# Optimization experiments

Hardware: AMD Instinct MI355X
Metric: run time of the kernel (lower is better)

The kernel has to match this reference:

```python
import jax, jax.numpy as jnp
import numpy as np
from jax import lax

B, T, H, W, C = 2, 32, 64, 64, 64
K, KT = 7, 5


def kernel_to_freq_3d(kernel, T, H, W):
    # kernel: (C, k_t, k_h, k_w) -> (C, T, H, W) complex freq (circularly centered)
    Cc, k_t, k_h, k_w = kernel.shape
    t_idx = (jnp.arange(k_t) - k_t // 2) % T
    h_idx = (jnp.arange(k_h) - k_h // 2) % H
    w_idx = (jnp.arange(k_w) - k_w // 2) % W
    tt, th, tw = jnp.meshgrid(t_idx, h_idx, w_idx, indexing='ij')
    padded = jnp.zeros((Cc, T, H, W), dtype=kernel.dtype).at[:, tt, th, tw].set(kernel)
    return jnp.fft.fftn(padded, axes=(1, 2, 3))


def heinsen_scan_log(log_coeffs, log_values):
    def op(left, right):
        a_l, b_l = left
        a_r, b_r = right
        return (a_l + a_r, jnp.logaddexp(a_r + b_l, b_r))
    _, log_h = lax.associative_scan(op, (log_coeffs, log_values), axis=0)
    return log_h


def setup_inputs() -> dict:
    key = jax.random.key(0)
    ks = jax.random.split(key, 9)
    dense_scale = 1.0 / np.sqrt(C)
    kern_scale = 1.0 / np.sqrt(KT * K * K)
    return {
        'x': jax.random.normal(ks[0], (B, T, H, W, C), jnp.float32),
        'gate_w': jax.random.normal(ks[1], (C, C), jnp.float32) * dense_scale,
        'gate_b': jnp.zeros((C,), jnp.float32),
        'hidden_w': jax.random.normal(ks[2], (C, C), jnp.float32) * dense_scale,
        'hidden_b': jnp.zeros((C,), jnp.float32),
        'gate_kernel': jax.random.normal(ks[3], (C, KT, K, K), jnp.float32) * kern_scale,
        'hidden_kernel': jax.random.normal(ks[4], (C, KT, K, K), jnp.float32) * kern_scale,
        'out_w': jax.random.normal(ks[5], (C, C), jnp.float32) * dense_scale,
        'out_b': jnp.zeros((C,), jnp.float32),
    }


def reference(x, gate_w, gate_b, hidden_w, hidden_b, gate_kernel, hidden_kernel, out_w, out_b):
    Bx, Tx, Hx, Wx, Cx = x.shape
    gate_proj = jnp.einsum('bthwc,cd->bthwd', x, gate_w) + gate_b
    hidden_proj = jnp.einsum('bthwc,cd->bthwd', x, hidden_w) + hidden_b
    # kernels to frequency domain, channel-last: (T, H, W, C)
    gk_f = kernel_to_freq_3d(gate_kernel, Tx, Hx, Wx).transpose(1, 2, 3, 0)
    hk_f = kernel_to_freq_3d(hidden_kernel, Tx, Hx, Wx).transpose(1, 2, 3, 0)
    gate_f = jnp.fft.fftn(gate_proj, axes=(1, 2, 3))
    hidden_f = jnp.fft.fftn(hidden_proj, axes=(1, 2, 3))
    gate_spatial = jnp.fft.ifftn(gate_f * gk_f[None], axes=(1, 2, 3)).real
    hidden_spatial = jnp.fft.ifftn(hidden_f * hk_f[None], axes=(1, 2, 3)).real
    # minGRU in log space: h_t = (1-z_t) h_{t-1} + z_t * h~_t
    log_forget = -jax.nn.softplus(gate_spatial)       # log(1 - z)
    log_update = -jax.nn.softplus(-gate_spatial)      # log(z)
    log_hidden = jnp.log(hidden_spatial ** 2 + 1e-06)
    log_values = log_update + log_hidden
    # scan over T (move T to axis 0)
    log_h_seq = heinsen_scan_log(
        log_forget.transpose(1, 0, 2, 3, 4), log_values.transpose(1, 0, 2, 3, 4))
    h = jnp.exp(log_h_seq.transpose(1, 0, 2, 3, 4))
    out = jnp.einsum('bthwc,cd->bthwd', h, out_w) + out_b
    return out.astype(jnp.float32)
```

## Files before the change

### kernel.cpp

```cpp
#include <hip/hip_runtime.h>
#include <hip/hip_fp16.h>

#define NELEM 16777216

typedef _Float16 f16x8 __attribute__((ext_vector_type(8)));
typedef _Float16 h2v  __attribute__((ext_vector_type(2)));
typedef float f32x4 __attribute__((ext_vector_type(4)));

static __device__ __forceinline__ void pk_fma_sv(uint& d, uint a_s, uint b_v) {
    asm("v_pk_fma_f16 %0, %1, %2, %0" : "+v"(d) : "s"(a_s), "v"(b_v));
}

__global__ __launch_bounds__(256) void proj2_kernel(
    const float* __restrict__ x,
    const float* __restrict__ wg, const float* __restrict__ bg,
    const float* __restrict__ wh, const float* __restrict__ bh,
    uint* __restrict__ pg, uint* __restrict__ ph)
{
    __shared__ __align__(16) _Float16 sX[128 * 64];
    __shared__ __align__(16) _Float16 sWT[2][64 * 64];
    const int tid = threadIdx.x;
    const int row0 = (int)blockIdx.x * 128;

    #pragma unroll
    for (int kci = 0; kci < 4; ++kci) {
        const int chunk = tid + kci * 256;
        const int r = chunk >> 3, q = chunk & 7;
        const float* gp = x + (long long)(row0 + r) * 64 + q * 8;
        const float4 v0 = *reinterpret_cast<const float4*>(gp);
        const float4 v1 = *reinterpret_cast<const float4*>(gp + 4);
        f16x8 hv;
        hv[0] = (_Float16)v0.x; hv[1] = (_Float16)v0.y; hv[2] = (_Float16)v0.z; hv[3] = (_Float16)v0.w;
        hv[4] = (_Float16)v1.x; hv[5] = (_Float16)v1.y; hv[6] = (_Float16)v1.z; hv[7] = (_Float16)v1.w;
        *reinterpret_cast<f16x8*>(&sX[r * 64 + ((q ^ (r & 7)) * 8)]) = hv;
    }
    {
        const int d = tid & 63;
        const int cb = (tid >> 6) * 16;
        #pragma unroll
        for (int i = 0; i < 16; ++i) {
            const int c = cb + i;
            const int off = d * 64 + (((c >> 3) ^ (d & 7)) * 8) + (c & 7);
            sWT[0][off] = (_Float16)wg[c * 64 + d];
            sWT[1][off] = (_Float16)wh[c * 64 + d];
        }
    }
    __syncthreads();

    const int wv = tid >> 6, lm = tid & 15, lg = (tid & 63) >> 4;
    f16x8 bf[2][4][2];
    #pragma unroll
    for (int nt = 0; nt < 4; ++nt) {
        const int d = nt * 16 + lm;
        #pragma unroll
        for (int s = 0; s < 2; ++s) {
            const int off = d * 64 + (((s * 4 + lg) ^ (d & 7)) * 8);
            bf[0][nt][s] = *reinterpret_cast<const f16x8*>(&sWT[0][off]);
            bf[1][nt][s] = *reinterpret_cast<const f16x8*>(&sWT[1][off]);
        }
    }
    f32x4 acc[2][2][4];
    #pragma unroll
    for (int m = 0; m < 2; ++m)
        #pragma unroll
        for (int mt = 0; mt < 2; ++mt)
            #pragma unroll
            for (int nt = 0; nt < 4; ++nt)
                acc[m][mt][nt] = (f32x4){0.f, 0.f, 0.f, 0.f};

    #pragma unroll
    for (int mt = 0; mt < 2; ++mt) {
        const int r = wv * 32 + mt * 16 + lm;
        const f16x8 a0 = *reinterpret_cast<const f16x8*>(&sX[r * 64 + ((lg ^ (r & 7)) * 8)]);
        const f16x8 a1 = *reinterpret_cast<const f16x8*>(&sX[r * 64 + (((4 + lg) ^ (r & 7)) * 8)]);
        #pragma unroll
        for (int nt = 0; nt < 4; ++nt) {
            acc[0][mt][nt] = __builtin_amdgcn_mfma_f32_16x16x32_f16(a0, bf[0][nt][0], acc[0][mt][nt], 0, 0, 0);
            acc[0][mt][nt] = __builtin_amdgcn_mfma_f32_16x16x32_f16(a1, bf[0][nt][1], acc[0][mt][nt], 0, 0, 0);
            acc[1][mt][nt] = __builtin_amdgcn_mfma_f32_16x16x32_f16(a0, bf[1][nt][0], acc[1][mt][nt], 0, 0, 0);
            acc[1][mt][nt] = __builtin_amdgcn_mfma_f32_16x16x32_f16(a1, bf[1][nt][1], acc[1][mt][nt], 0, 0, 0);
        }
    }
    #pragma unroll
    for (int nt = 0; nt < 4; ++nt) {
        const int col = nt * 16 + lm;
        const int pr  = col >> 1;
        const float bgv = bg[col], bhv = bh[col];
        #pragma unroll
        for (int mt = 0; mt < 2; ++mt) {
            const int rb = row0 + wv * 32 + mt * 16 + lg * 4;
            uint pk0[4], pk1[4];
            #pragma unroll
            for (int i = 0; i < 4; ++i) {
                const float v0 = acc[0][mt][nt][i] + bgv;
                const float p0 = __shfl_xor(v0, 1);
                const float v1 = acc[1][mt][nt][i] + bhv;
                const float p1 = __shfl_xor(v1, 1);
                h2v a, c;
                a[0] = (_Float16)((lm & 1) ? p0 : v0); a[1] = (_Float16)((lm & 1) ? v0 : p0);
                c[0] = (_Float16)((lm & 1) ? p1 : v1); c[1] = (_Float16)((lm & 1) ? v1 : p1);
                pk0[i] = __builtin_bit_cast(uint, a);
                pk1[i] = __builtin_bit_cast(uint, c);
            }
            if (!(lm & 1)) {
                *reinterpret_cast<uint4*>(pg + pr * 262144 + rb) = make_uint4(pk0[0], pk0[1], pk0[2], pk0[3]);
                *reinterpret_cast<uint4*>(ph + pr * 262144 + rb) = make_uint4(pk1[0], pk1[1], pk1[2], pk1[3]);
            }
        }
    }
}

__global__ __launch_bounds__(256) void tapconv_kernel(
    const float* __restrict__ gk, const float* __restrict__ hk, uint* __restrict__ taps)
{
    const int i = blockIdx.x * 256 + threadIdx.x;
    if (i >= 17920) return;
    const int kw = i & 7;
    int r = i >> 3;
    const int kth = r % 35;  r /= 35;
    const int p = r & 31;
    const int mat = r >> 5;
    if (kw >= 7) { taps[i] = 0u; return; }
    const float* K = mat ? hk : gk;
    const int tap = kth * 7 + kw;
    h2v hv;
    hv[0] = (_Float16)K[(2 * p) * 245 + tap];
    hv[1] = (_Float16)K[(2 * p + 1) * 245 + tap];
    taps[i] = __builtin_bit_cast(uint, hv);
}

__global__ __launch_bounds__(256) void conv3d_dual_kernel(
    const uint* __restrict__ inG, uint* __restrict__ outG,
    const uint* __restrict__ inH, uint* __restrict__ outH,
    const uint* __restrict__ taps)
{
    const int bid = (int)blockIdx.x;
    const int l = ((bid & 7) << 9) | (bid >> 3);
    const int tile = l & 3;
    const int pgrp = (l >> 2) & 7;
    const int t    = (l >> 5) & 31;
    const int b    = (l >> 10) & 1;
    const int mat  = (l >> 11) & 1;
    const int wave = threadIdx.x >> 6;
    const int lane = threadIdx.x & 63;
    const int h0 = (tile >> 1) * 32, w0 = (tile & 1) * 32;
    const int pair = pgrp * 4 + wave;

    const uint* in = mat ? inH : inG;
    uint* out      = mat ? outH : outG;

    const int iy = lane >> 3, ix = lane & 7;

    const int tapOff = __builtin_amdgcn_readfirstlane((mat * 32 + pair) * 280);
    const uint* tb = taps + tapOff;
    const int pbOff = __builtin_amdgcn_readfirstlane(pair * 262144 + b * 131072);

    int colu[3];
    #pragma unroll
    for (int m = 0; m < 3; ++m) colu[m] = (w0 + 4 * ix - 4 + 4 * m) & 63;

    uint tot[4][4];
    #pragma unroll
    for (int o = 0; o < 4; ++o)
        #pragma unroll
        for (int j = 0; j < 4; ++j) tot[o][j] = 0u;

    #pragma unroll 1
    for (int kt = 0; kt < 5; ++kt) {
        const int tin = (t - kt + 2) & 31;
        const uint* pin = in + pbOff + tin * 4096;
        const uint* tkt = tb + kt * 56;

        uint kv[7][8];
        #pragma unroll
        for (int kh = 6; kh >= 5; --kh)
            #pragma unroll
            for (int i2 = 0; i2 < 8; ++i2) kv[kh][i2] = tkt[kh * 8 + i2];

        #pragma unroll
        for (int rr = 0; rr < 10; ++rr) {
            if (rr <= 4) {
                const int kh = 4 - rr;
                #pragma unroll
                for (int i2 = 0; i2 < 8; ++i2) kv[kh][i2] = tkt[kh * 8 + i2];
            }
            const int gh = (h0 - 3 + 4 * iy + rr) & 63;
            const int rowu = gh * 64;
            uint row[12];
            #pragma unroll
            for (int m = 0; m < 3; ++m) {
                const uint4 v = *reinterpret_cast<const uint4*>(pin + rowu + colu[m]);
                row[4 * m]     = v.x; row[4 * m + 1] = v.y;
                row[4 * m + 2] = v.z; row[4 * m + 3] = v.w;
            }
            #pragma unroll
            for (int o = 0; o < 4; ++o) {
                const int kh = o + 6 - rr;
                if (kh < 0 || kh > 6) continue;
                #pragma unroll
                for (int kw = 0; kw < 7; ++kw)
                    #pragma unroll
                    for (int j = 0; j < 4; ++j)
                        pk_fma_sv(tot[o][j], kv[kh][kw], row[j + 7 - kw]);
            }
        }
    }

    uint* ob = out + pair * 262144 + (b * 32 + t) * 4096;
    #pragma unroll
    for (int o = 0; o < 4; ++o)
        *reinterpret_cast<uint4*>(ob + (h0 + 4 * iy + o) * 64 + (w0 + 4 * ix)) =
            make_uint4(tot[o][0], tot[o][1], tot[o][2], tot[o][3]);
}

__global__ __launch_bounds__(256) void scan_kernel(
    const uint* __restrict__ gs, const uint* __restrict__ hs, uint* __restrict__ hout)
{
    const int tid = blockIdx.x * 256 + threadIdx.x;
    const int base = (tid >> 12) * 131072 + (tid & 4095);
    float h0 = 0.f, h1 = 0.f;
    for (int t = 0; t < 32; ++t) {
        const int a = base + t * 4096;
        const float2 g  = __half22float2(__builtin_bit_cast(__half2, gs[a]));
        const float2 hv = __half22float2(__builtin_bit_cast(__half2, hs[a]));
        const float z0 = 1.f / (1.f + __expf(-g.x));
        const float z1 = 1.f / (1.f + __expf(-g.y));
        h0 = fmaf(1.f - z0, h0, z0 * fmaf(hv.x, hv.x, 1e-6f));
        h1 = fmaf(1.f - z1, h1, z1 * fmaf(hv.y, hv.y, 1e-6f));
        hout[a] = __builtin_bit_cast(uint, __floats2half2_rn(h0, h1));
    }
}

__global__ __launch_bounds__(256) void outgemm_kernel(
    const uint* __restrict__ hin, const float* __restrict__ w,
    const float* __restrict__ bias, float* __restrict__ out)
{
    __shared__ __align__(16) uint sXu[128 * 36];
    __shared__ __align__(16) _Float16 sWT[64 * 64];
    const int tid = threadIdx.x;
    const int row0 = (int)blockIdx.x * 128;

    {
        const int pr = tid >> 3, k = tid & 7;
        const uint* src = hin + pr * 262144 + row0 + k * 16;
        #pragma unroll
        for (int q = 0; q < 4; ++q) {
            const uint4 v = *reinterpret_cast<const uint4*>(src + q * 4);
            sXu[(k * 16 + q * 4 + 0) * 36 + pr] = v.x;
            sXu[(k * 16 + q * 4 + 1) * 36 + pr] = v.y;
            sXu[(k * 16 + q * 4 + 2) * 36 + pr] = v.z;
            sXu[(k * 16 + q * 4 + 3) * 36 + pr] = v.w;
        }
    }
    {
        const int d = tid & 63;
        const int cb = (tid >> 6) * 16;
        #pragma unroll
        for (int i = 0; i < 16; ++i) {
            const int c = cb + i;
            sWT[d * 64 + (((c >> 3) ^ (d & 7)) * 8) + (c & 7)] = (_Float16)w[c * 64 + d];
        }
    }
    __syncthreads();

    const int wv = tid >> 6, lm = tid & 15, lg = (tid & 63) >> 4;
    f16x8 bf[4][2];
    #pragma unroll
    for (int nt = 0; nt < 4; ++nt) {
        const int d = nt * 16 + lm;
        #pragma unroll
        for (int s = 0; s < 2; ++s)
            bf[nt][s] = *reinterpret_cast<const f16x8*>(&sWT[d * 64 + (((s * 4 + lg) ^ (d & 7)) * 8)]);
    }
    f32x4 acc[2][4];
    #pragma unroll
    for (int mt = 0; mt < 2; ++mt)
        #pragma unroll
        for (int nt = 0; nt < 4; ++nt)
            acc[mt][nt] = (f32x4){0.f, 0.f, 0.f, 0.f};

    #pragma unroll
    for (int mt = 0; mt < 2; ++mt) {
        const int r = wv * 32 + mt * 16 + lm;
        const f16x8 a0 = *reinterpret_cast<const f16x8*>(&sXu[r * 36 + lg * 4]);
        const f16x8 a1 = *reinterpret_cast<const f16x8*>(&sXu[r * 36 + 16 + lg * 4]);
        #pragma unroll
        for (int nt = 0; nt < 4; ++nt) {
            acc[mt][nt] = __builtin_amdgcn_mfma_f32_16x16x32_f16(a0, bf[nt][0], acc[mt][nt], 0, 0, 0);
            acc[mt][nt] = __builtin_amdgcn_mfma_f32_16x16x32_f16(a1, bf[nt][1], acc[mt][nt], 0, 0, 0);
        }
    }
    #pragma unroll
    for (int nt = 0; nt < 4; ++nt) {
        const int col = nt * 16 + lm;
        const float bv = bias[col];
        #pragma unroll
        for (int mt = 0; mt < 2; ++mt) {
            const long long rb = row0 + wv * 32 + mt * 16 + lg * 4;
            #pragma unroll
            for (int i = 0; i < 4; ++i)
                out[(rb + i) * 64 + col] = acc[mt][nt][i] + bv;
        }
    }
}

extern "C" void kernel_launch(void* const* d_in, const int* in_sizes, int n_in,
                              void* d_out, int out_size, void* d_ws, size_t ws_size,
                              hipStream_t stream)
{
    const float* x  = (const float*)d_in[0];
    const float* gw = (const float*)d_in[1];
    const float* gb = (const float*)d_in[2];
    const float* hw = (const float*)d_in[3];
    const float* hb = (const float*)d_in[4];
    const float* gk = (const float*)d_in[5];
    const float* hk = (const float*)d_in[6];
    const float* ow = (const float*)d_in[7];
    const float* ob = (const float*)d_in[8];

    uint* W1 = (uint*)d_ws;
    uint* W2 = W1 + NELEM / 2;
    uint* W3 = W2 + NELEM / 2;
    uint* taps = W3 + NELEM / 2;
    uint* Dsc = (uint*)d_out;

    tapconv_kernel<<<70, 256, 0, stream>>>(gk, hk, taps);
    proj2_kernel<<<2048, 256, 0, stream>>>(x, gw, gb, hw, hb, W1, W2);
    conv3d_dual_kernel<<<4096, 256, 0, stream>>>(W1, W3, W2, Dsc, taps);
    scan_kernel<<<1024, 256, 0, stream>>>(W3, Dsc, W1);
    outgemm_kernel<<<2048, 256, 0, stream>>>(W1, ow, ob, (float*)d_out);
}
```

Baseline: 207.6 us.

## Stage conv input rows into per-wave LDS slab with full-width 16-row tiles

The depthwise 3D conv kernel now copies the 24 input rows (including halo) needed for each temporal tap into a per-wave LDS slab. The inner loop then reads from LDS instead of issuing repeated global loads. Tiles change from 32x32 to 16 rows by full 64-column width, and the block index mapping is reordered. All 7 kernel-row taps are preloaded up front and the kw/o loop order is swapped. The 66-word row stride makes 16-byte LDS accesses misaligned on odd rows, and preloading all taps raises register pressure.

```diff
diff --git a/kernel.cpp b/kernel.cpp
--- a/kernel.cpp
+++ b/kernel.cpp
@@ -134,30 +134,44 @@
     const uint* __restrict__ inH, uint* __restrict__ outH,
     const uint* __restrict__ taps)
 {
+    __shared__ __align__(16) uint slabAll[4 * 1584];
+
     const int bid = (int)blockIdx.x;
     const int l = ((bid & 7) << 9) | (bid >> 3);
-    const int tile = l & 3;
-    const int pgrp = (l >> 2) & 7;
-    const int t    = (l >> 5) & 31;
+    const int hb   = l & 3;
+    const int t    = (l >> 2) & 31;
+    const int pgrp = (l >> 7) & 7;
     const int b    = (l >> 10) & 1;
     const int mat  = (l >> 11) & 1;
     const int wave = threadIdx.x >> 6;
     const int lane = threadIdx.x & 63;
-    const int h0 = (tile >> 1) * 32, w0 = (tile & 1) * 32;
+    const int h0 = hb * 16;
     const int pair = pgrp * 4 + wave;
 
     const uint* in = mat ? inH : inG;
     uint* out      = mat ? outH : outG;
-
-    const int iy = lane >> 3, ix = lane & 7;
+    uint* slab = slabAll + wave * 1584;
+
+    const int iy = lane >> 4, ix = lane & 15;
 
     const int tapOff = __builtin_amdgcn_readfirstlane((mat * 32 + pair) * 280);
     const uint* tb = taps + tapOff;
     const int pbOff = __builtin_amdgcn_readfirstlane(pair * 262144 + b * 131072);
 
+    const int srow = lane >> 4;
+    const int sc4  = lane & 15;
+    int gsrc[6], ldst[6];
+    #pragma unroll
+    for (int i = 0; i < 6; ++i) {
+        const int r = 4 * i + srow;
+        const int gh = (h0 - 3 + r) & 63;
+        gsrc[i] = gh * 64 + 4 * sc4;
+        ldst[i] = r * 66 + 4 * sc4;
+    }
+
     int colu[3];
     #pragma unroll
-    for (int m = 0; m < 3; ++m) colu[m] = (w0 + 4 * ix - 4 + 4 * m) & 63;
+    for (int m = 0; m < 3; ++m) colu[m] = (4 * ix - 4 + 4 * m) & 63;
 
     uint tot[4][4];
     #pragma unroll
@@ -173,43 +187,45 @@
 
         uint kv[7][8];
         #pragma unroll
-        for (int kh = 6; kh >= 5; --kh)
+        for (int kh = 0; kh < 7; ++kh)
             #pragma unroll
             for (int i2 = 0; i2 < 8; ++i2) kv[kh][i2] = tkt[kh * 8 + i2];
 
+        uint4 st[6];
+        #pragma unroll
+        for (int i = 0; i < 6; ++i)
+            st[i] = *reinterpret_cast<const uint4*>(pin + gsrc[i]);
+        #pragma unroll
+        for (int i = 0; i < 6; ++i)
+            *reinterpret_cast<uint4*>(slab + ldst[i]) = st[i];
+
         #pragma unroll
         for (int rr = 0; rr < 10; ++rr) {
-            if (rr <= 4) {
-                const int kh = 4 - rr;
-                #pragma unroll
-                for (int i2 = 0; i2 < 8; ++i2) kv[kh][i2] = tkt[kh * 8 + i2];
-            }
-            const int gh = (h0 - 3 + 4 * iy + rr) & 63;
-            const int rowu = gh * 64;
+            const uint* rp = slab + (4 * iy + rr) * 66;
             uint row[12];
             #pragma unroll
             for (int m = 0; m < 3; ++m) {
-                const uint4 v = *reinterpret_cast<const uint4*>(pin + rowu + colu[m]);
+                const uint4 v = *reinterpret_cast<const uint4*>(rp + colu[m]);
                 row[4 * m]     = v.x; row[4 * m + 1] = v.y;
                 row[4 * m + 2] = v.z; row[4 * m + 3] = v.w;
             }
             #pragma unroll
-            for (int o = 0; o < 4; ++o) {
-                const int kh = o + 6 - rr;
-                if (kh < 0 || kh > 6) continue;
+            for (int kw = 0; kw < 7; ++kw)
                 #pragma unroll
-                for (int kw = 0; kw < 7; ++kw)
+                for (int o = 0; o < 4; ++o) {
+                    const int kh = o + 6 - rr;
+                    if (kh < 0 || kh > 6) continue;
                     #pragma unroll
                     for (int j = 0; j < 4; ++j)
                         pk_fma_sv(tot[o][j], kv[kh][kw], row[j + 7 - kw]);
-            }
-        }
-    }
-
-    uint* ob = out + pair * 262144 + (b * 32 + t) * 4096;
+                }
+        }
+    }
+
+    uint* ob = out + pair * 262144 + (b * 32 + t) * 4096 + h0 * 64;
     #pragma unroll
     for (int o = 0; o < 4; ++o)
-        *reinterpret_cast<uint4*>(ob + (h0 + 4 * iy + o) * 64 + (w0 + 4 * ix)) =
+        *reinterpret_cast<uint4*>(ob + (4 * iy + o) * 64 + 4 * ix) =
             make_uint4(tot[o][0], tot[o][1], tot[o][2], tot[o][3]);
 }
 
```

Measured after the change: 243.1 us. 1.17x slower.

## Compute two output time steps per block in 3D conv to reuse input slices

Applied to the files above, without the earlier changes.

Each conv block now produces two consecutive time outputs, iterating over six input time slices instead of five per output. Each loaded input row feeds both accumulators: one uses scalar taps and the other uses taps carried over in vector registers from the previous step. The aim is to cut redundant global loads of input slices and halve the grid. In exchange, register pressure rises sharply (56 vector tap registers plus a second accumulator set), which could lower occupancy or cause spills.

```diff
diff --git a/kernel.cpp b/kernel.cpp
--- a/kernel.cpp
+++ b/kernel.cpp
@@ -9,6 +9,9 @@
 
 static __device__ __forceinline__ void pk_fma_sv(uint& d, uint a_s, uint b_v) {
     asm("v_pk_fma_f16 %0, %1, %2, %0" : "+v"(d) : "s"(a_s), "v"(b_v));
+}
+static __device__ __forceinline__ void pk_fma_vv(uint& d, uint a_v, uint b_v) {
+    asm("v_pk_fma_f16 %0, %1, %2, %0" : "+v"(d) : "v"(a_v), "v"(b_v));
 }
 
 __global__ __launch_bounds__(256) void proj2_kernel(
@@ -135,15 +138,16 @@
     const uint* __restrict__ taps)
 {
     const int bid = (int)blockIdx.x;
-    const int l = ((bid & 7) << 9) | (bid >> 3);
+    const int l = ((bid & 7) << 8) | (bid >> 3);
     const int tile = l & 3;
     const int pgrp = (l >> 2) & 7;
-    const int t    = (l >> 5) & 31;
-    const int b    = (l >> 10) & 1;
-    const int mat  = (l >> 11) & 1;
+    const int tp   = (l >> 5) & 15;
+    const int b    = (l >> 9) & 1;
+    const int mat  = (l >> 10) & 1;
     const int wave = threadIdx.x >> 6;
     const int lane = threadIdx.x & 63;
     const int h0 = (tile >> 1) * 32, w0 = (tile & 1) * 32;
+    const int t0 = tp * 2;
     const int pair = pgrp * 4 + wave;
 
     const uint* in = mat ? inH : inG;
@@ -158,59 +162,78 @@
     int colu[3];
     #pragma unroll
     for (int m = 0; m < 3; ++m) colu[m] = (w0 + 4 * ix - 4 + 4 * m) & 63;
-
-    uint tot[4][4];
+    int rowu[10];
+    #pragma unroll
+    for (int rr = 0; rr < 10; ++rr) rowu[rr] = ((h0 - 3 + 4 * iy + rr) & 63) * 64;
+
+    uint tot0[4][4], tot1[4][4];
     #pragma unroll
     for (int o = 0; o < 4; ++o)
         #pragma unroll
-        for (int j = 0; j < 4; ++j) tot[o][j] = 0u;
+        for (int j = 0; j < 4; ++j) { tot0[o][j] = 0u; tot1[o][j] = 0u; }
+
+    uint kvS[56];
+    uint kvV[56];
 
     #pragma unroll 1
-    for (int kt = 0; kt < 5; ++kt) {
-        const int tin = (t - kt + 2) & 31;
+    for (int e = 0; e < 6; ++e) {
+        if (e > 0) {
+            #pragma unroll
+            for (int i = 0; i < 56; ++i) kvV[i] = kvS[i];
+        }
+        if (e <= 4) {
+            const uint* tkt = tb + (4 - e) * 56;
+            #pragma unroll
+            for (int i = 0; i < 56; ++i) kvS[i] = tkt[i];
+        }
+
+        const int tin = (t0 - 2 + e) & 31;
         const uint* pin = in + pbOff + tin * 4096;
-        const uint* tkt = tb + kt * 56;
-
-        uint kv[7][8];
-        #pragma unroll
-        for (int kh = 6; kh >= 5; --kh)
-            #pragma unroll
-            for (int i2 = 0; i2 < 8; ++i2) kv[kh][i2] = tkt[kh * 8 + i2];
 
         #pragma unroll
         for (int rr = 0; rr < 10; ++rr) {
-            if (rr <= 4) {
-                const int kh = 4 - rr;
-                #pragma unroll
-                for (int i2 = 0; i2 < 8; ++i2) kv[kh][i2] = tkt[kh * 8 + i2];
-            }
-            const int gh = (h0 - 3 + 4 * iy + rr) & 63;
-            const int rowu = gh * 64;
             uint row[12];
             #pragma unroll
             for (int m = 0; m < 3; ++m) {
-                const uint4 v = *reinterpret_cast<const uint4*>(pin + rowu + colu[m]);
+                const uint4 v = *reinterpret_cast<const uint4*>(pin + rowu[rr] + colu[m]);
                 row[4 * m]     = v.x; row[4 * m + 1] = v.y;
                 row[4 * m + 2] = v.z; row[4 * m + 3] = v.w;
             }
-            #pragma unroll
-            for (int o = 0; o < 4; ++o) {
-                const int kh = o + 6 - rr;
-                if (kh < 0 || kh > 6) continue;
+            if (e <= 4) {
                 #pragma unroll
                 for (int kw = 0; kw < 7; ++kw)
                     #pragma unroll
-                    for (int j = 0; j < 4; ++j)
-                        pk_fma_sv(tot[o][j], kv[kh][kw], row[j + 7 - kw]);
-            }
-        }
-    }
-
-    uint* ob = out + pair * 262144 + (b * 32 + t) * 4096;
-    #pragma unroll
-    for (int o = 0; o < 4; ++o)
-        *reinterpret_cast<uint4*>(ob + (h0 + 4 * iy + o) * 64 + (w0 + 4 * ix)) =
-            make_uint4(tot[o][0], tot[o][1], tot[o][2], tot[o][3]);
+                    for (int o = 0; o < 4; ++o) {
+                        const int kh = o + 6 - rr;
+                        if (kh < 0 || kh > 6) continue;
+                        #pragma unroll
+                        for (int j = 0; j < 4; ++j)
+                            pk_fma_sv(tot0[o][j], kvS[kh * 8 + kw], row[j + 7 - kw]);
+                    }
+            }
+            if (e >= 1) {
+                #pragma unroll
+                for (int kw = 0; kw < 7; ++kw)
+                    #pragma unroll
+                    for (int o = 0; o < 4; ++o) {
+                        const int kh = o + 6 - rr;
+                        if (kh < 0 || kh > 6) continue;
+                        #pragma unroll
+                        for (int j = 0; j < 4; ++j)
+                            pk_fma_vv(tot1[o][j], kvV[kh * 8 + kw], row[j + 7 - kw]);
+                    }
+            }
+        }
+    }
+
+    uint* ob0 = out + pair * 262144 + (b * 32 + t0) * 4096;
+    #pragma unroll
+    for (int o = 0; o < 4; ++o) {
+        *reinterpret_cast<uint4*>(ob0 + (h0 + 4 * iy + o) * 64 + (w0 + 4 * ix)) =
+            make_uint4(tot0[o][0], tot0[o][1], tot0[o][2], tot0[o][3]);
+        *reinterpret_cast<uint4*>(ob0 + 4096 + (h0 + 4 * iy + o) * 64 + (w0 + 4 * ix)) =
+            make_uint4(tot1[o][0], tot1[o][1], tot1[o][2], tot1[o][3]);
+    }
 }
 
 __global__ __launch_bounds__(256) void scan_kernel(
@@ -326,7 +349,7 @@
 
     tapconv_kernel<<<70, 256, 0, stream>>>(gk, hk, taps);
     proj2_kernel<<<2048, 256, 0, stream>>>(x, gw, gb, hw, hb, W1, W2);
-    conv3d_dual_kernel<<<4096, 256, 0, stream>>>(W1, W3, W2, Dsc, taps);
+    conv3d_dual_kernel<<<2048, 256, 0, stream>>>(W1, W3, W2, Dsc, taps);
     scan_kernel<<<1024, 256, 0, stream>>>(W3, Dsc, W1);
     outgemm_kernel<<<2048, 256, 0, stream>>>(W1, ow, ob, (float*)d_out);
 }
```

After: 239.0 us. +15.1%, slower.
